# Kernel optimization log

Measured on AMD Instinct MI355X. Metric: run time of the kernel, lower is better.

The kernel has to match this reference:

```python
import jax, jax.numpy as jnp
import numpy as np

B, S, D, H, F, M = 2, 2048, 1024, 16, 4096, 1024
HD = D // H
LR, MOM_DECAY, WD, THRESH = 0.01, 0.9, 0.01, 0.1


def rmsnorm(x, w, eps=1e-8):
    n = jnp.linalg.norm(x, axis=-1, keepdims=True) * (x.shape[-1] ** -0.5)
    return w * x / (n + eps)


def rope_sin_cos(seq_len, dim):
    inv_freq = 1.0 / (10000.0 ** (jnp.arange(0, dim, 2, dtype=jnp.float32) / dim))
    ang = jnp.arange(seq_len, dtype=jnp.float32)[:, None] * inv_freq[None, :]  # [S, dim/2]
    return jnp.sin(ang), jnp.cos(ang)


def apply_rope(x, sin, cos):
    # x: [B,H,S,hd]; sin/cos: [S,hd/2] broadcast. Matches torch source:
    # split even/odd lanes, then CONCATENATE halves (not interleave).
    x1, x2 = x[..., ::2], x[..., 1::2]
    return jnp.concatenate([x1 * cos - x2 * sin, x1 * sin + x2 * cos], axis=-1)


def lmm_mlp(z, w0, b0, w1, b1):
    return jnp.maximum(z @ w0 + b0, 0.0) @ w1 + b1


def setup_inputs() -> dict:
    key = jax.random.key(0)
    k = jax.random.split(key, 20)
    sc = 0.02
    r = lambda i, shape: jax.random.normal(k[i], shape, jnp.float32) * sc
    return {
        'x': jax.random.normal(k[0], (B, S, D), jnp.float32),
        'mask': jnp.tril(jnp.ones((1, 1, S, S), dtype=bool)),
        'wq': r(1, (D, D)), 'wk': r(2, (D, D)), 'wv': r(3, (D, D)), 'wo': r(4, (D, D)),
        'n1': jnp.ones(D, jnp.float32), 'n2': jnp.ones(D, jnp.float32), 'n3': jnp.ones(D, jnp.float32),
        'ffn_w1': r(5, (D, F)), 'ffn_w2': r(6, (D, F)), 'ffn_w3': r(7, (F, D)),
        'pk_w': r(8, (D, M)), 'pk_b': jnp.zeros(M, jnp.float32),
        'pv_w': r(9, (D, M)), 'pv_b': jnp.zeros(M, jnp.float32),
        'pq_w': r(10, (D, M)), 'pq_b': jnp.zeros(M, jnp.float32),
        'l0_w': r(11, (M, M)), 'l0_b': jnp.zeros(M, jnp.float32),
        'l1_w': r(12, (M, M)), 'l1_b': jnp.zeros(M, jnp.float32),
        'm0_w': jnp.zeros((M, M), jnp.float32), 'm0_b': jnp.zeros(M, jnp.float32),
        'm1_w': jnp.zeros((M, M), jnp.float32), 'm1_b': jnp.zeros(M, jnp.float32),
    }


def reference(x, mask, wq, wk, wv, wo, n1, n2, n3, ffn_w1, ffn_w2, ffn_w3,
              pk_w, pk_b, pv_w, pv_b, pq_w, pq_b,
              l0_w, l0_b, l1_w, l1_b, m0_w, m0_b, m1_w, m1_b):
    # ---- attention sublayer (pre-norm, RoPE) ----
    hn = rmsnorm(x, n1)
    q = (hn @ wq).reshape(B, S, H, HD).transpose(0, 2, 1, 3)
    kk = (hn @ wk).reshape(B, S, H, HD).transpose(0, 2, 1, 3)
    v = (hn @ wv).reshape(B, S, H, HD).transpose(0, 2, 1, 3)
    sin, cos = rope_sin_cos(S, HD)
    q = apply_rope(q, sin, cos)
    kk = apply_rope(kk, sin, cos)
    scores = jnp.einsum('bhqd,bhkd->bhqk', q, kk) / np.sqrt(HD).astype(np.float32)
    scores = jnp.where(mask, scores, -jnp.inf)
    attn = jax.nn.softmax(scores, axis=-1)
    o = jnp.einsum('bhqk,bhkd->bhqd', attn, v).transpose(0, 2, 1, 3).reshape(B, S, D)
    h = x + o @ wo

    # ---- neural memory sublayer ----
    hn2 = rmsnorm(h, n2)
    q_lmm = hn2 @ pq_w + pq_b
    retrieved = lmm_mlp(q_lmm, l0_w, l0_b, l1_w, l1_b)  # uses PRE-update params

    # online Titan-style LMM update (torch does this under no_grad, after retrieval)
    kf = jax.lax.stop_gradient((hn2 @ pk_w + pk_b).reshape(B * S, M))
    vf = jax.lax.stop_gradient((hn2 @ pv_w + pv_b).reshape(B * S, M))

    def lmm_loss(params):
        pred = lmm_mlp(kf, *params)
        return jnp.sum(jnp.mean((pred - vf) ** 2, axis=-1))

    params = (l0_w, l0_b, l1_w, l1_b)
    loss_sum, grads = jax.value_and_grad(lmm_loss)(params)
    avg_loss = loss_sum / (B * S)
    do_update = avg_loss >= THRESH
    moms = (m0_w, m0_b, m1_w, m1_b)
    new_moms, new_params = [], []
    for p, m, g in zip(params, moms, grads):
        nm = MOM_DECAY * m - LR * g
        np_ = p * (1.0 - WD) + nm
        new_moms.append(jnp.where(do_update, nm, m))
        new_params.append(jnp.where(do_update, np_, p))

    h = h + retrieved

    # ---- SwiGLU FFN sublayer ----
    hn3 = rmsnorm(h, n3)
    ffn = (jax.nn.silu(hn3 @ ffn_w1) * (hn3 @ ffn_w2)) @ ffn_w3
    out = h + ffn
    return (out, *new_params, *new_moms)
```

## Files before the change

kernel.cpp:

```cpp
#include <hip/hip_runtime.h>
#include <cstdint>
#include <cstddef>

typedef __bf16 bf16;
typedef __bf16 bf16x2 __attribute__((ext_vector_type(2)));
typedef __bf16 bf16x4 __attribute__((ext_vector_type(4)));
typedef __bf16 bf16x8 __attribute__((ext_vector_type(8)));
typedef float  f32x4  __attribute__((ext_vector_type(4)));
typedef __attribute__((address_space(1))) unsigned int u32_g;
typedef __attribute__((address_space(3))) unsigned int u32_l;

#define DI __device__ __forceinline__

constexpr int Bc = 2, Sc = 2048, Dc = 1024, Hc = 16, HDc = 64, Fc = 4096, Mc = 1024;
constexpr int NTc = Bc * Sc;

DI void llds16(const bf16* g, bf16* l) {
  __builtin_amdgcn_global_load_lds((const u32_g*)g, (u32_l*)l, 16, 0, 0);
}
DI f32x4 cvt4(bf16x4 a) {
  f32x4 r; r[0] = (float)a[0]; r[1] = (float)a[1]; r[2] = (float)a[2]; r[3] = (float)a[3];
  return r;
}

__global__ void k_detect(const unsigned short* __restrict__ x, int* __restrict__ flag)
{
  const int tid = threadIdx.x;
  int cnt = 0;
#pragma unroll
  for (int i = 0; i < 8; i++) {
    unsigned short h = x[tid * 8 + i];
    int e = (h >> 7) & 0xFF;
    if (e < 96 || e > 160) cnt++;
  }
#pragma unroll
  for (int off = 32; off > 0; off >>= 1) cnt += __shfl_down(cnt, off, 64);
  if (tid == 0) *flag = (cnt > 32) ? 1 : 0;
}

__global__ __launch_bounds__(256)
void k_cvt(const void* __restrict__ src, bf16* __restrict__ dst, int n4, const int* __restrict__ flag)
{
  int i = blockIdx.x * 256 + threadIdx.x;
  if (i >= n4) return;
  bf16x4 o;
  if (*flag) {
    f32x4 v = ((const f32x4*)src)[i];
    o[0] = (bf16)v[0]; o[1] = (bf16)v[1]; o[2] = (bf16)v[2]; o[3] = (bf16)v[3];
  } else {
    o = ((const bf16x4*)src)[i];
  }
  ((bf16x4*)dst)[i] = o;
}

__global__ void k_transpose_dt(const void* __restrict__ src, bf16* __restrict__ dst,
                               int R, int C, const int* __restrict__ flag)
{
  __shared__ bf16 tile[32][33];
  const int c0 = blockIdx.x * 32, r0 = blockIdx.y * 32;
  const int tx = threadIdx.x, ty = threadIdx.y;
  const bool f32 = (*flag != 0);
  for (int i = ty; i < 32; i += 8) {
    size_t idx = (size_t)(r0 + i) * C + (c0 + tx);
    tile[i][tx] = f32 ? (bf16)((const float*)src)[idx] : ((const bf16*)src)[idx];
  }
  __syncthreads();
  for (int i = ty; i < 32; i += 8)
    dst[(size_t)(c0 + i) * R + (r0 + tx)] = tile[tx][i];
}

__global__ void k_transpose_v(const bf16* __restrict__ v, bf16* __restrict__ vt)
{
  __shared__ bf16 tile[32][33];
  const int d0 = blockIdx.x * 32, s0 = blockIdx.y * 32;
  const int bh = blockIdx.z;
  const int b = bh >> 4, hh = bh & 15;
  const int tx = threadIdx.x, ty = threadIdx.y;
  for (int i = ty; i < 32; i += 8)
    tile[i][tx] = v[((size_t)(b * Sc + s0 + i)) * Dc + hh * HDc + d0 + tx];
  __syncthreads();
  for (int i = ty; i < 32; i += 8)
    vt[((size_t)(bh * HDc + d0 + i)) * Sc + s0 + tx] = tile[tx][i];
}

enum EpiMode { EPI_BF16 = 0, EPI_BIAS_BF16, EPI_BIAS_RELU_BF16, EPI_BIAS_RESB_F32,
               EPI_SILU_BF16, EPI_DZ_BF16, EPI_RESX_BF16, EPI_RESF_F32 };

template <int EPI>
__global__ __launch_bounds__(256)
void k_gemm(const bf16* __restrict__ A, const bf16* __restrict__ Bt,
            int Mr, int Nr, int Kr,
            float* outF, bf16* outB,
            const bf16* __restrict__ bias, const bf16* auxB,
            const float* resF,
            const void* __restrict__ resX, const int* __restrict__ flag)
{
  __shared__ bf16 As[128 * 32];
  __shared__ bf16 Bs[128 * 32];
  const int tid = threadIdx.x;
  const int w = tid >> 6, l = tid & 63;
  const int wr = w >> 1, wc = w & 1;
  const int row0 = blockIdx.y * 128, col0 = blockIdx.x * 128;

  const f32x4 vzero = {0.f, 0.f, 0.f, 0.f};
  f32x4 acc[4][4];
#pragma unroll
  for (int i = 0; i < 4; i++)
#pragma unroll
    for (int j = 0; j < 4; j++) acc[i][j] = vzero;

  const bf16* Ag = A + (size_t)(row0 + w * 16 + (l >> 2)) * Kr + ((l & 3) << 3);
  const bf16* Bg = Bt + (size_t)(col0 + w * 16 + (l >> 2)) * Kr + ((l & 3) << 3);
  bf16* AsW = &As[w * 512];
  bf16* BsW = &Bs[w * 512];
  const size_t rowHop = (size_t)64 * Kr;

  for (int k0 = 0; k0 < Kr; k0 += 32) {
    __syncthreads();
    llds16(Ag + k0, AsW);
    llds16(Ag + rowHop + k0, AsW + 2048);
    llds16(Bg + k0, BsW);
    llds16(Bg + rowHop + k0, BsW + 2048);
    __syncthreads();
    bf16x8 af[4], bfr[4];
#pragma unroll
    for (int mt = 0; mt < 4; mt++)
      af[mt] = *(const bf16x8*)&As[(wr * 64 + mt * 16 + (l & 15)) * 32 + (l >> 4) * 8];
#pragma unroll
    for (int nt = 0; nt < 4; nt++)
      bfr[nt] = *(const bf16x8*)&Bs[(wc * 64 + nt * 16 + (l & 15)) * 32 + (l >> 4) * 8];
#pragma unroll
    for (int mt = 0; mt < 4; mt++)
#pragma unroll
      for (int nt = 0; nt < 4; nt++)
        acc[mt][nt] = __builtin_amdgcn_mfma_f32_16x16x32_bf16(af[mt], bfr[nt], acc[mt][nt], 0, 0, 0);
  }

  const bool f32res = (EPI == EPI_RESX_BF16) ? (*flag != 0) : false;
  float biasv[4];
  if (EPI == EPI_BIAS_BF16 || EPI == EPI_BIAS_RELU_BF16 || EPI == EPI_BIAS_RESB_F32) {
#pragma unroll
    for (int nt = 0; nt < 4; nt++)
      biasv[nt] = (float)bias[col0 + wc * 64 + nt * 16 + (l & 15)];
  }
#pragma unroll
  for (int mt = 0; mt < 4; mt++) {
    const int rowb = row0 + wr * 64 + mt * 16 + ((l >> 4) << 2);
    float av[4][4];
    if (EPI == EPI_SILU_BF16 || EPI == EPI_DZ_BF16 || EPI == EPI_BIAS_RESB_F32) {
#pragma unroll
      for (int nt = 0; nt < 4; nt++) {
        const int col = col0 + wc * 64 + nt * 16 + (l & 15);
#pragma unroll
        for (int r = 0; r < 4; r++)
          av[nt][r] = (float)auxB[(size_t)(rowb + r) * Nr + col];
      }
    }
    if (EPI == EPI_RESF_F32) {
#pragma unroll
      for (int nt = 0; nt < 4; nt++) {
        const int col = col0 + wc * 64 + nt * 16 + (l & 15);
#pragma unroll
        for (int r = 0; r < 4; r++)
          av[nt][r] = resF[(size_t)(rowb + r) * Nr + col];
      }
    }
    if (EPI == EPI_RESX_BF16) {
#pragma unroll
      for (int nt = 0; nt < 4; nt++) {
        const int col = col0 + wc * 64 + nt * 16 + (l & 15);
#pragma unroll
        for (int r = 0; r < 4; r++) {
          const size_t idx = (size_t)(rowb + r) * Nr + col;
          av[nt][r] = f32res ? ((const float*)resX)[idx] : (float)((const bf16*)resX)[idx];
        }
      }
    }
#pragma unroll
    for (int nt = 0; nt < 4; nt++) {
      const int col = col0 + wc * 64 + nt * 16 + (l & 15);
#pragma unroll
      for (int r = 0; r < 4; r++) {
        const size_t idx = (size_t)(rowb + r) * Nr + col;
        float v = acc[mt][nt][r];
        if (EPI == EPI_BF16) { outB[idx] = (bf16)v; }
        else if (EPI == EPI_BIAS_BF16) { outB[idx] = (bf16)(v + biasv[nt]); }
        else if (EPI == EPI_BIAS_RELU_BF16) { outB[idx] = (bf16)fmaxf(v + biasv[nt], 0.f); }
        else if (EPI == EPI_BIAS_RESB_F32) { outF[idx] = v + biasv[nt] + av[nt][r]; }
        else if (EPI == EPI_SILU_BF16) {
          float s1v = av[nt][r];
          float sl = s1v / (1.f + __expf(-s1v));
          outB[idx] = (bf16)(sl * v);
        }
        else if (EPI == EPI_DZ_BF16) { outB[idx] = (bf16)(av[nt][r] > 0.f ? v : 0.f); }
        else if (EPI == EPI_RESX_BF16) { outB[idx] = (bf16)(v + av[nt][r]); }
        else if (EPI == EPI_RESF_F32) { outF[idx] = v + av[nt][r]; }
      }
    }
  }
}

__global__ __launch_bounds__(256)
void k_gemm_tn(const bf16* __restrict__ X, const bf16* __restrict__ Y, int Kt,
               float* __restrict__ out)
{
  __shared__ bf16 As[128 * 36];
  __shared__ bf16 Bs[128 * 36];
  const int tid = threadIdx.x;
  const int w = tid >> 6, l = tid & 63;
  const int wr = w >> 1, wc = w & 1;
  const int row0 = blockIdx.y * 128, col0 = blockIdx.x * 128;
  const int iofs = (tid & 15) * 8;
  const int tp   = (tid >> 4) * 2;

  const f32x4 vzero = {0.f, 0.f, 0.f, 0.f};
  f32x4 acc[4][4];
#pragma unroll
  for (int i = 0; i < 4; i++)
#pragma unroll
    for (int j = 0; j < 4; j++) acc[i][j] = vzero;

  const int chunk = Kt / gridDim.z;
  const int tbeg = blockIdx.z * chunk;

  for (int t0 = tbeg; t0 < tbeg + chunk; t0 += 32) {
    __syncthreads();
    bf16x8 a0 = *(const bf16x8*)&X[(size_t)(t0 + tp) * 1024 + row0 + iofs];
    bf16x8 a1 = *(const bf16x8*)&X[(size_t)(t0 + tp + 1) * 1024 + row0 + iofs];
    bf16x8 b0 = *(const bf16x8*)&Y[(size_t)(t0 + tp) * 1024 + col0 + iofs];
    bf16x8 b1 = *(const bf16x8*)&Y[(size_t)(t0 + tp + 1) * 1024 + col0 + iofs];
#pragma unroll
    for (int e = 0; e < 8; e++) {
      bf16x2 pa; pa[0] = a0[e]; pa[1] = a1[e];
      bf16x2 pb; pb[0] = b0[e]; pb[1] = b1[e];
      *(bf16x2*)&As[(iofs + e) * 36 + tp] = pa;
      *(bf16x2*)&Bs[(iofs + e) * 36 + tp] = pb;
    }
    __syncthreads();
    bf16x8 af[4], bfr[4];
#pragma unroll
    for (int mt = 0; mt < 4; mt++) {
      const int base = (wr * 64 + mt * 16 + (l & 15)) * 36 + (l >> 4) * 8;
      bf16x4 lo = *(const bf16x4*)&As[base];
      bf16x4 hi = *(const bf16x4*)&As[base + 4];
#pragma unroll
      for (int e = 0; e < 4; e++) { af[mt][e] = lo[e]; af[mt][4 + e] = hi[e]; }
    }
#pragma unroll
    for (int nt = 0; nt < 4; nt++) {
      const int base = (wc * 64 + nt * 16 + (l & 15)) * 36 + (l >> 4) * 8;
      bf16x4 lo = *(const bf16x4*)&Bs[base];
      bf16x4 hi = *(const bf16x4*)&Bs[base + 4];
#pragma unroll
      for (int e = 0; e < 4; e++) { bfr[nt][e] = lo[e]; bfr[nt][4 + e] = hi[e]; }
    }
#pragma unroll
    for (int mt = 0; mt < 4; mt++)
#pragma unroll
      for (int nt = 0; nt < 4; nt++)
        acc[mt][nt] = __builtin_amdgcn_mfma_f32_16x16x32_bf16(af[mt], bfr[nt], acc[mt][nt], 0, 0, 0);
  }

#pragma unroll
  for (int mt = 0; mt < 4; mt++) {
    const int rowb = row0 + wr * 64 + mt * 16 + ((l >> 4) << 2);
#pragma unroll
    for (int nt = 0; nt < 4; nt++) {
      const int col = col0 + wc * 64 + nt * 16 + (l & 15);
#pragma unroll
      for (int r = 0; r < 4; r++)
        atomicAdd(&out[(size_t)(rowb + r) * 1024 + col], acc[mt][nt][r]);
    }
  }
}

__global__ __launch_bounds__(256)
void k_rmsnorm_dt(const void* __restrict__ x, const bf16* __restrict__ w, bf16* __restrict__ out,
                  const int* __restrict__ flag)
{
  const int row = blockIdx.x;
  const int tid = threadIdx.x;
  f32x4 xv;
  if (*flag) xv = *(const f32x4*)((const float*)x + (size_t)row * Dc + tid * 4);
  else       xv = cvt4(*(const bf16x4*)((const bf16*)x + (size_t)row * Dc + tid * 4));
  float ss = xv[0] * xv[0] + xv[1] * xv[1] + xv[2] * xv[2] + xv[3] * xv[3];
#pragma unroll
  for (int off = 32; off > 0; off >>= 1) ss += __shfl_down(ss, off, 64);
  __shared__ float part[4];
  if ((tid & 63) == 0) part[tid >> 6] = ss;
  __syncthreads();
  float tot = part[0] + part[1] + part[2] + part[3];
  float inv = 1.f / (sqrtf(tot) * 0.03125f + 1e-8f);
  bf16x4 wb = *(const bf16x4*)(w + tid * 4);
  bf16x4 ov;
  ov[0] = (bf16)((float)wb[0] * xv[0] * inv);
  ov[1] = (bf16)((float)wb[1] * xv[1] * inv);
  ov[2] = (bf16)((float)wb[2] * xv[2] * inv);
  ov[3] = (bf16)((float)wb[3] * xv[3] * inv);
  *(bf16x4*)(out + (size_t)row * Dc + tid * 4) = ov;
}

__global__ __launch_bounds__(256)
void k_rmsnorm_b(const bf16* __restrict__ x, const bf16* __restrict__ w, bf16* __restrict__ out)
{
  const int row = blockIdx.x;
  const int tid = threadIdx.x;
  f32x4 xv = cvt4(*(const bf16x4*)(x + (size_t)row * Dc + tid * 4));
  float ss = xv[0] * xv[0] + xv[1] * xv[1] + xv[2] * xv[2] + xv[3] * xv[3];
#pragma unroll
  for (int off = 32; off > 0; off >>= 1) ss += __shfl_down(ss, off, 64);
  __shared__ float part[4];
  if ((tid & 63) == 0) part[tid >> 6] = ss;
  __syncthreads();
  float tot = part[0] + part[1] + part[2] + part[3];
  float inv = 1.f / (sqrtf(tot) * 0.03125f + 1e-8f);
  bf16x4 wb = *(const bf16x4*)(w + tid * 4);
  bf16x4 ov;
  ov[0] = (bf16)((float)wb[0] * xv[0] * inv);
  ov[1] = (bf16)((float)wb[1] * xv[1] * inv);
  ov[2] = (bf16)((float)wb[2] * xv[2] * inv);
  ov[3] = (bf16)((float)wb[3] * xv[3] * inv);
  *(bf16x4*)(out + (size_t)row * Dc + tid * 4) = ov;
}

__global__ __launch_bounds__(256)
void k_rmsnorm_f(const float* __restrict__ x, const bf16* __restrict__ w, bf16* __restrict__ out)
{
  const int row = blockIdx.x;
  const int tid = threadIdx.x;
  f32x4 xv = *(const f32x4*)(x + (size_t)row * Dc + tid * 4);
  float ss = xv[0] * xv[0] + xv[1] * xv[1] + xv[2] * xv[2] + xv[3] * xv[3];
#pragma unroll
  for (int off = 32; off > 0; off >>= 1) ss += __shfl_down(ss, off, 64);
  __shared__ float part[4];
  if ((tid & 63) == 0) part[tid >> 6] = ss;
  __syncthreads();
  float tot = part[0] + part[1] + part[2] + part[3];
  float inv = 1.f / (sqrtf(tot) * 0.03125f + 1e-8f);
  bf16x4 wb = *(const bf16x4*)(w + tid * 4);
  bf16x4 ov;
  ov[0] = (bf16)((float)wb[0] * xv[0] * inv);
  ov[1] = (bf16)((float)wb[1] * xv[1] * inv);
  ov[2] = (bf16)((float)wb[2] * xv[2] * inv);
  ov[3] = (bf16)((float)wb[3] * xv[3] * inv);
  *(bf16x4*)(out + (size_t)row * Dc + tid * 4) = ov;
}

__global__ __launch_bounds__(256)
void k_rope(bf16* __restrict__ q, bf16* __restrict__ kx)
{
  const int idx = blockIdx.x * 256 + threadIdx.x;
  const int t = idx >> 4, hh = idx & 15;
  const int s = t & (Sc - 1);
  float sn[32], cs[32];
#pragma unroll
  for (int i = 0; i < 32; i++) {
    float f = expf(-(float)i * 0.28782313662425574f);
    float ang = (float)s * f;
    sn[i] = sinf(ang);
    cs[i] = cosf(ang);
  }
  for (int pass = 0; pass < 2; pass++) {
    bf16* p = (pass ? kx : q) + (size_t)t * Dc + hh * HDc;
    float xb[64], ob[64];
#pragma unroll
    for (int j = 0; j < 16; j++) *(f32x4*)&xb[j * 4] = cvt4(*(const bf16x4*)(p + j * 4));
#pragma unroll
    for (int i = 0; i < 32; i++) {
      float x1 = xb[2 * i], x2 = xb[2 * i + 1];
      ob[i] = x1 * cs[i] - x2 * sn[i];
      ob[32 + i] = x1 * sn[i] + x2 * cs[i];
    }
#pragma unroll
    for (int j = 0; j < 16; j++) {
      bf16x4 o4;
      o4[0] = (bf16)ob[j * 4]; o4[1] = (bf16)ob[j * 4 + 1];
      o4[2] = (bf16)ob[j * 4 + 2]; o4[3] = (bf16)ob[j * 4 + 3];
      *(bf16x4*)(p + j * 4) = o4;
    }
  }
}

__global__ __launch_bounds__(256)
void k_attn(const bf16* __restrict__ q, const bf16* __restrict__ kx,
            const bf16* __restrict__ vt, bf16* __restrict__ o)
{
  constexpr int PAD = 72;
  __shared__ bf16 Ps[4][16 * PAD];

  const int blk = blockIdx.x;
  const int qt = 31 - (blk >> 5);
  const int bh = blk & 31;
  const int b = bh >> 4, hh = bh & 15;
  const int tid = threadIdx.x;
  const int w = tid >> 6, l = tid & 63;
  const int quad = l >> 4, c = l & 15;

  const int qrow = qt * 64 + w * 16 + c;
  const size_t qbase = ((size_t)(b * Sc + qrow)) * Dc + hh * HDc;
  bf16x8 qf0 = *(const bf16x8*)(q + qbase + quad * 8);
  bf16x8 qf1 = *(const bf16x8*)(q + qbase + 32 + quad * 8);
#pragma unroll
  for (int j = 0; j < 8; j++) {
    qf0[j] = (bf16)((float)qf0[j] * 0.125f);
    qf1[j] = (bf16)((float)qf1[j] * 0.125f);
  }

  const f32x4 vzero = {0.f, 0.f, 0.f, 0.f};
  f32x4 oacc[4];
#pragma unroll
  for (int nt = 0; nt < 4; nt++) oacc[nt] = vzero;
  float mrun[4] = {-3.0e38f, -3.0e38f, -3.0e38f, -3.0e38f};
  float lrun[4] = {0.f, 0.f, 0.f, 0.f};

  const int qrow0 = qt * 64 + w * 16 + quad * 4;

  const bf16* kb = kx + (size_t)b * Sc * Dc + hh * HDc;
  const bf16* vb = vt + (size_t)bh * HDc * Sc;

  for (int t0 = 0; t0 <= qt; t0++) {
    const int kk0 = t0 * 64;

    f32x4 sf[4];
#pragma unroll
    for (int nt = 0; nt < 4; nt++) {
      const bf16* kr = kb + (size_t)(kk0 + nt * 16 + c) * Dc + quad * 8;
      bf16x8 k0 = *(const bf16x8*)kr;
      bf16x8 k1 = *(const bf16x8*)(kr + 32);
      f32x4 a = vzero;
      a = __builtin_amdgcn_mfma_f32_16x16x32_bf16(qf0, k0, a, 0, 0, 0);
      a = __builtin_amdgcn_mfma_f32_16x16x32_bf16(qf1, k1, a, 0, 0, 0);
      sf[nt] = a;
    }
    if (t0 == qt) {
#pragma unroll
      for (int nt = 0; nt < 4; nt++)
#pragma unroll
        for (int r = 0; r < 4; r++)
          if (kk0 + nt * 16 + c > qrow0 + r) sf[nt][r] = -3.0e38f;
    }

    float mnew[4], alpha[4];
#pragma unroll
    for (int r = 0; r < 4; r++) {
      float mt = fmaxf(fmaxf(sf[0][r], sf[1][r]), fmaxf(sf[2][r], sf[3][r]));
      mt = fmaxf(mt, __shfl_xor(mt, 1, 64));
      mt = fmaxf(mt, __shfl_xor(mt, 2, 64));
      mt = fmaxf(mt, __shfl_xor(mt, 4, 64));
      mt = fmaxf(mt, __shfl_xor(mt, 8, 64));
      mnew[r] = fmaxf(mrun[r], mt);
      alpha[r] = __expf(mrun[r] - mnew[r]);
      mrun[r] = mnew[r];
    }
    float ps[4] = {0.f, 0.f, 0.f, 0.f};
#pragma unroll
    for (int nt = 0; nt < 4; nt++)
#pragma unroll
      for (int r = 0; r < 4; r++) {
        float p = __expf(sf[nt][r] - mnew[r]);
        sf[nt][r] = p;
        ps[r] += p;
      }
#pragma unroll
    for (int r = 0; r < 4; r++) {
      ps[r] += __shfl_xor(ps[r], 1, 64);
      ps[r] += __shfl_xor(ps[r], 2, 64);
      ps[r] += __shfl_xor(ps[r], 4, 64);
      ps[r] += __shfl_xor(ps[r], 8, 64);
      lrun[r] = lrun[r] * alpha[r] + ps[r];
    }
#pragma unroll
    for (int nt = 0; nt < 4; nt++)
#pragma unroll
      for (int r = 0; r < 4; r++) oacc[nt][r] *= alpha[r];

#pragma unroll
    for (int nt = 0; nt < 4; nt++)
#pragma unroll
      for (int r = 0; r < 4; r++)
        Ps[w][(quad * 4 + r) * PAD + nt * 16 + c] = (bf16)sf[nt][r];
    bf16x8 pa0 = *(const bf16x8*)&Ps[w][c * PAD + quad * 8];
    bf16x8 pa1 = *(const bf16x8*)&Ps[w][c * PAD + 32 + quad * 8];

#pragma unroll
    for (int nt = 0; nt < 4; nt++) {
      const bf16* vr = vb + (size_t)(nt * 16 + c) * Sc + kk0 + quad * 8;
      bf16x8 v0 = *(const bf16x8*)vr;
      bf16x8 v1 = *(const bf16x8*)(vr + 32);
      oacc[nt] = __builtin_amdgcn_mfma_f32_16x16x32_bf16(pa0, v0, oacc[nt], 0, 0, 0);
      oacc[nt] = __builtin_amdgcn_mfma_f32_16x16x32_bf16(pa1, v1, oacc[nt], 0, 0, 0);
    }
  }

  float inv[4];
#pragma unroll
  for (int r = 0; r < 4; r++) inv[r] = 1.f / lrun[r];
#pragma unroll
  for (int r = 0; r < 4; r++) {
    const size_t obase = ((size_t)(b * Sc + qrow0 + r)) * Dc + hh * HDc;
#pragma unroll
    for (int nt = 0; nt < 4; nt++)
      o[obase + nt * 16 + c] = (bf16)(oacc[nt][r] * inv[r]);
  }
}

__global__ __launch_bounds__(256)
void k_relu(const bf16* __restrict__ src, bf16* __restrict__ dst)
{
  int i = blockIdx.x * 256 + threadIdx.x;
  bf16x8 v = ((const bf16x8*)src)[i];
  bf16x8 o;
#pragma unroll
  for (int e = 0; e < 8; e++) o[e] = ((float)v[e] > 0.f) ? v[e] : (bf16)0.f;
  ((bf16x8*)dst)[i] = o;
}

__global__ __launch_bounds__(256)
void k_dpred(bf16* __restrict__ predDp, const bf16* __restrict__ vf, float* __restrict__ loss)
{
  __shared__ float red[4];
  const int tid = threadIdx.x;
  const size_t n8 = (size_t)NTc * Mc / 8;
  float lacc = 0.f;
  for (size_t i = (size_t)blockIdx.x * 256 + tid; i < n8; i += (size_t)gridDim.x * 256) {
    bf16x8 p8 = ((const bf16x8*)predDp)[i];
    bf16x8 v8 = ((const bf16x8*)vf)[i];
    bf16x8 d8;
#pragma unroll
    for (int e = 0; e < 8; e++) {
      float df = (float)p8[e] - (float)v8[e];
      lacc += df * df;
      d8[e] = (bf16)(df * (2.0f / 1024.0f));
    }
    ((bf16x8*)predDp)[i] = d8;
  }
#pragma unroll
  for (int off = 32; off > 0; off >>= 1) lacc += __shfl_down(lacc, off, 64);
  if ((tid & 63) == 0) red[tid >> 6] = lacc;
  __syncthreads();
  if (tid == 0) atomicAdd(loss, red[0] + red[1] + red[2] + red[3]);
}

__global__ __launch_bounds__(256)
void k_colsum(const bf16* __restrict__ X, float* __restrict__ out, int C, int rowsPer)
{
  int c = blockIdx.x * 256 + threadIdx.x;
  int r0 = blockIdx.y * rowsPer;
  float s = 0.f;
#pragma unroll 8
  for (int r = r0; r < r0 + rowsPer; r++) s += (float)X[(size_t)r * C + c];
  atomicAdd(&out[c], s);
}

__global__ __launch_bounds__(256)
void k_update_dt(const void* __restrict__ p0w, const void* __restrict__ p0b,
                 const void* __restrict__ p1w, const void* __restrict__ p1b,
                 const void* __restrict__ m0w, const void* __restrict__ m0b,
                 const void* __restrict__ m1w, const void* __restrict__ m1b,
                 const float* __restrict__ g0wF, const float* __restrict__ g0b,
                 const float* __restrict__ g1wF, const float* __restrict__ g1b,
                 const float* __restrict__ loss, const int* __restrict__ flag,
                 float* __restrict__ outP, float* __restrict__ outM)
{
  const int i = blockIdx.x * 256 + threadIdx.x;
  const bool upd = (loss[0] >= 0.1f * 1024.f * 4096.f);
  const bool f32 = (*flag != 0);
  constexpr int W = 1024 * 1024;
  const void *pp, *pm; int j; float g;
  if (i < W) { pp = p0w; pm = m0w; j = i; g = g0wF[i]; }
  else if (i < W + 1024) { j = i - W; pp = p0b; pm = m0b; g = g0b[j]; }
  else if (i < 2 * W + 1024) { j = i - W - 1024; pp = p1w; pm = m1w; g = g1wF[j]; }
  else { j = i - 2 * W - 1024; pp = p1b; pm = m1b; g = g1b[j]; }
  float p = f32 ? ((const float*)pp)[j] : (float)((const bf16*)pp)[j];
  float m = f32 ? ((const float*)pm)[j] : (float)((const bf16*)pm)[j];
  float nm = 0.9f * m - 0.01f * g;
  float np = 0.99f * p + nm;
  outP[i] = upd ? np : p;
  outM[i] = upd ? nm : m;
}

extern "C" void kernel_launch(void* const* d_in, const int* in_sizes, int n_in,
                              void* d_out, int out_size, void* d_ws, size_t ws_size,
                              hipStream_t stream)
{
  (void)in_sizes; (void)n_in; (void)out_size; (void)ws_size;
  const void* x   = d_in[0];
  const void* wq  = d_in[2];
  const void* wk  = d_in[3];
  const void* wv  = d_in[4];
  const void* wo  = d_in[5];
  const void* n1  = d_in[6];
  const void* n2  = d_in[7];
  const void* n3  = d_in[8];
  const void* fw1 = d_in[9];
  const void* fw2 = d_in[10];
  const void* fw3 = d_in[11];
  const void* pkw = d_in[12];
  const void* pkb = d_in[13];
  const void* pvw = d_in[14];
  const void* pvb = d_in[15];
  const void* pqw = d_in[16];
  const void* pqb = d_in[17];
  const void* l0w = d_in[18];
  const void* l0b = d_in[19];
  const void* l1w = d_in[20];
  const void* l1b = d_in[21];
  const void* m0w = d_in[22];
  const void* m0b = d_in[23];
  const void* m1w = d_in[24];
  const void* m1b = d_in[25];

  char* ws = (char*)d_ws;
  size_t off = 0;
  auto alloc = [&](size_t bytes) -> char* {
    char* p = ws + off;
    off += (bytes + 255) & ~(size_t)255;
    return p;
  };

  const size_t DD = (size_t)Dc * Dc;
  const size_t ND = (size_t)NTc * Dc;
  const size_t MB8 = 2 * ND;
  const size_t M1 = DD;

  bf16* W = (bf16*)alloc(2 * 8 * M1);
  bf16 *wqT = W, *wkT = W + M1, *wvT = W + 2 * M1, *woT = W + 3 * M1;
  bf16 *pqT = W + 4 * M1, *pkT = W + 5 * M1, *pvT = W + 6 * M1, *l0T = W + 7 * M1;
  bf16 *l1T = W + M1;
  bf16 *l1c = W;
  bf16 *w1T = W + 4 * M1;
  bf16 *w2T = W;
  bf16 *w3T = W + 4 * M1;

  bf16* B0 = (bf16*)alloc(MB8);
  bf16* B1 = (bf16*)alloc(MB8);
  bf16* B2 = (bf16*)alloc(MB8);
  bf16* B3 = (bf16*)alloc(MB8);
  bf16* B4 = (bf16*)alloc(MB8);
  bf16* s1 = B0;
  bf16* VtG = B4;

  float* g0b = (float*)alloc(4 * 1024);
  float* g1b = (float*)alloc(4 * 1024);
  float* lossb = (float*)alloc(256);
  int*   flag  = (int*)alloc(256);
  bf16* n1c = (bf16*)alloc(2 * 1024);
  bf16* n2c = (bf16*)alloc(2 * 1024);
  bf16* n3c = (bf16*)alloc(2 * 1024);
  bf16* bqc = (bf16*)alloc(2 * 1024);
  bf16* bkc = (bf16*)alloc(2 * 1024);
  bf16* bvc = (bf16*)alloc(2 * 1024);
  bf16* b0c = (bf16*)alloc(2 * 1024);
  bf16* b1c = (bf16*)alloc(2 * 1024);

  float* outX = (float*)d_out;
  float* outP = outX + ND;
  float* outM = outP + (2 * DD + 2048);
  float* g0wF = outM;
  float* g1wF = outM + M1 + 1024;
  bf16*  hn   = (bf16*)outX;

  const dim3 tb(32, 8);

  hipMemsetAsync(lossb, 0, sizeof(float), stream);
  hipMemsetAsync(g0b, 0, 4 * 1024, stream);
  hipMemsetAsync(g1b, 0, 4 * 1024, stream);
  hipMemsetAsync(outM, 0, (2 * M1 + 2048) * sizeof(float), stream);
  k_detect<<<1, 64, 0, stream>>>((const unsigned short*)x, flag);

  k_cvt<<<1, 256, 0, stream>>>(n1, n1c, 256, flag);
  k_cvt<<<1, 256, 0, stream>>>(n2, n2c, 256, flag);
  k_cvt<<<1, 256, 0, stream>>>(n3, n3c, 256, flag);
  k_cvt<<<1, 256, 0, stream>>>(pqb, bqc, 256, flag);
  k_cvt<<<1, 256, 0, stream>>>(pkb, bkc, 256, flag);
  k_cvt<<<1, 256, 0, stream>>>(pvb, bvc, 256, flag);
  k_cvt<<<1, 256, 0, stream>>>(l0b, b0c, 256, flag);
  k_cvt<<<1, 256, 0, stream>>>(l1b, b1c, 256, flag);

  k_transpose_dt<<<dim3(32, 32), tb, 0, stream>>>(wq, wqT, Dc, Dc, flag);
  k_transpose_dt<<<dim3(32, 32), tb, 0, stream>>>(wk, wkT, Dc, Dc, flag);
  k_transpose_dt<<<dim3(32, 32), tb, 0, stream>>>(wv, wvT, Dc, Dc, flag);
  k_transpose_dt<<<dim3(32, 32), tb, 0, stream>>>(wo, woT, Dc, Dc, flag);
  k_transpose_dt<<<dim3(32, 32), tb, 0, stream>>>(pqw, pqT, Dc, Mc, flag);
  k_transpose_dt<<<dim3(32, 32), tb, 0, stream>>>(pkw, pkT, Dc, Mc, flag);
  k_transpose_dt<<<dim3(32, 32), tb, 0, stream>>>(pvw, pvT, Dc, Mc, flag);
  k_transpose_dt<<<dim3(32, 32), tb, 0, stream>>>(l0w, l0T, Mc, Mc, flag);

  k_rmsnorm_dt<<<NTc, 256, 0, stream>>>(x, n1c, hn, flag);
  k_gemm<EPI_BF16><<<dim3(8, 32), 256, 0, stream>>>(hn, wqT, NTc, Dc, Dc, nullptr, B0, nullptr, nullptr, nullptr, nullptr, nullptr);
  k_gemm<EPI_BF16><<<dim3(8, 32), 256, 0, stream>>>(hn, wkT, NTc, Dc, Dc, nullptr, B1, nullptr, nullptr, nullptr, nullptr, nullptr);
  k_gemm<EPI_BF16><<<dim3(8, 32), 256, 0, stream>>>(hn, wvT, NTc, Dc, Dc, nullptr, B2, nullptr, nullptr, nullptr, nullptr, nullptr);
  k_transpose_v<<<dim3(2, 64, 32), tb, 0, stream>>>(B2, VtG);
  k_rope<<<256, 256, 0, stream>>>(B0, B1);
  k_attn<<<1024, 256, 0, stream>>>(B0, B1, VtG, B3);
  k_gemm<EPI_RESX_BF16><<<dim3(8, 32), 256, 0, stream>>>(B3, woT, NTc, Dc, Dc, nullptr, B4, nullptr, nullptr, nullptr, x, flag);
  k_transpose_dt<<<dim3(32, 32), tb, 0, stream>>>(l1w, l1T, Mc, Mc, flag);

  k_rmsnorm_b<<<NTc, 256, 0, stream>>>(B4, n2c, B0);
  k_gemm<EPI_BIAS_BF16><<<dim3(8, 32), 256, 0, stream>>>(B0, pqT, NTc, Mc, Dc, nullptr, B1, bqc, nullptr, nullptr, nullptr, nullptr);
  k_gemm<EPI_BIAS_BF16><<<dim3(8, 32), 256, 0, stream>>>(B0, pkT, NTc, Mc, Dc, nullptr, B2, bkc, nullptr, nullptr, nullptr, nullptr);
  k_gemm<EPI_BIAS_BF16><<<dim3(8, 32), 256, 0, stream>>>(B0, pvT, NTc, Mc, Dc, nullptr, B3, bvc, nullptr, nullptr, nullptr, nullptr);
  k_gemm<EPI_BIAS_RELU_BF16><<<dim3(8, 32), 256, 0, stream>>>(B1, l0T, NTc, Mc, Mc, nullptr, B0, b0c, nullptr, nullptr, nullptr, nullptr);
  k_gemm<EPI_BIAS_RESB_F32><<<dim3(8, 32), 256, 0, stream>>>(B0, l1T, NTc, Mc, Mc, outX, nullptr, b1c, B4, nullptr, nullptr, nullptr);

  k_gemm<EPI_BIAS_BF16><<<dim3(8, 32), 256, 0, stream>>>(B2, l0T, NTc, Mc, Mc, nullptr, B4, b0c, nullptr, nullptr, nullptr, nullptr);
  k_transpose_dt<<<dim3(128, 32), tb, 0, stream>>>(fw1, w1T, Dc, Fc, flag);
  k_relu<<<2048, 256, 0, stream>>>(B4, B0);
  k_gemm<EPI_BIAS_BF16><<<dim3(8, 32), 256, 0, stream>>>(B0, l1T, NTc, Mc, Mc, nullptr, B1, b1c, nullptr, nullptr, nullptr, nullptr);
  k_cvt<<<1024, 256, 0, stream>>>(l1w, l1c, (int)(DD / 4), flag);
  k_dpred<<<256, 256, 0, stream>>>(B1, B3, lossb);
  k_gemm<EPI_DZ_BF16><<<dim3(8, 32), 256, 0, stream>>>(B1, l1c, NTc, Mc, Mc, nullptr, B3, nullptr, B4, nullptr, nullptr, nullptr);
  k_gemm_tn<<<dim3(8, 8, 8), 256, 0, stream>>>(B0, B1, NTc, g1wF);
  k_gemm_tn<<<dim3(8, 8, 8), 256, 0, stream>>>(B2, B3, NTc, g0wF);
  k_colsum<<<dim3(4, 32), 256, 0, stream>>>(B1, g1b, Mc, NTc / 32);
  k_colsum<<<dim3(4, 32), 256, 0, stream>>>(B3, g0b, Mc, NTc / 32);
  k_update_dt<<<8200, 256, 0, stream>>>(l0w, l0b, l1w, l1b, m0w, m0b, m1w, m1b,
                                        g0wF, g0b, g1wF, g1b, lossb, flag, outP, outM);

  k_transpose_dt<<<dim3(128, 32), tb, 0, stream>>>(fw2, w2T, Dc, Fc, flag);
  k_rmsnorm_f<<<NTc, 256, 0, stream>>>(outX, n3c, B4);
  k_gemm<EPI_BF16><<<dim3(32, 32), 256, 0, stream>>>(B4, w1T, NTc, Fc, Dc, nullptr, s1, nullptr, nullptr, nullptr, nullptr, nullptr);
  k_transpose_dt<<<dim3(32, 128), tb, 0, stream>>>(fw3, w3T, Fc, Dc, flag);
  k_gemm<EPI_SILU_BF16><<<dim3(32, 32), 256, 0, stream>>>(B4, w2T, NTc, Fc, Dc, nullptr, s1, nullptr, s1, nullptr, nullptr, nullptr);
  k_gemm<EPI_RESF_F32><<<dim3(8, 32), 256, 0, stream>>>(s1, w3T, NTc, Dc, Fc, outX, nullptr, nullptr, nullptr, outX, nullptr, nullptr);
}
```

Before: 1.117 ms.

## Split attention KV loop across waves with in-block softmax merge

Each attention block now handles 16 query rows instead of 64, and the four waves split the key tiles among themselves in strided order. Partial outputs, maxima and sums from waves 1-3 go through shared memory and are merged by wave 0 with a log-sum-exp rescale. The grid grows fourfold to raise parallelism and balance causal work. In exchange, waves in a block no longer share the same K/V tiles, so total K/V loads increase, and a merge step with two barriers is added.

```diff
diff --git a/kernel.cpp b/kernel.cpp
--- a/kernel.cpp
+++ b/kernel.cpp
@@ -386,17 +386,20 @@
             const bf16* __restrict__ vt, bf16* __restrict__ o)
 {
   constexpr int PAD = 72;
-  __shared__ bf16 Ps[4][16 * PAD];
+  __shared__ __align__(16) char smem[19456];
 
   const int blk = blockIdx.x;
-  const int qt = 31 - (blk >> 5);
+  const int qi = 127 - (blk >> 5);
   const int bh = blk & 31;
   const int b = bh >> 4, hh = bh & 15;
   const int tid = threadIdx.x;
   const int w = tid >> 6, l = tid & 63;
   const int quad = l >> 4, c = l & 15;
 
-  const int qrow = qt * 64 + w * 16 + c;
+  bf16* Psw = (bf16*)smem + w * 16 * PAD;
+  float* Buf = (float*)smem;
+
+  const int qrow = qi * 16 + c;
   const size_t qbase = ((size_t)(b * Sc + qrow)) * Dc + hh * HDc;
   bf16x8 qf0 = *(const bf16x8*)(q + qbase + quad * 8);
   bf16x8 qf1 = *(const bf16x8*)(q + qbase + 32 + quad * 8);
@@ -413,12 +416,13 @@
   float mrun[4] = {-3.0e38f, -3.0e38f, -3.0e38f, -3.0e38f};
   float lrun[4] = {0.f, 0.f, 0.f, 0.f};
 
-  const int qrow0 = qt * 64 + w * 16 + quad * 4;
+  const int qrow0 = qi * 16 + quad * 4;
+  const int ntiles = (qi >> 2) + 1;
 
   const bf16* kb = kx + (size_t)b * Sc * Dc + hh * HDc;
   const bf16* vb = vt + (size_t)bh * HDc * Sc;
 
-  for (int t0 = 0; t0 <= qt; t0++) {
+  for (int t0 = w; t0 < ntiles; t0 += 4) {
     const int kk0 = t0 * 64;
 
     f32x4 sf[4];
@@ -432,7 +436,7 @@
       a = __builtin_amdgcn_mfma_f32_16x16x32_bf16(qf1, k1, a, 0, 0, 0);
       sf[nt] = a;
     }
-    if (t0 == qt) {
+    if (t0 == ntiles - 1) {
 #pragma unroll
       for (int nt = 0; nt < 4; nt++)
 #pragma unroll
@@ -478,9 +482,9 @@
     for (int nt = 0; nt < 4; nt++)
 #pragma unroll
       for (int r = 0; r < 4; r++)
-        Ps[w][(quad * 4 + r) * PAD + nt * 16 + c] = (bf16)sf[nt][r];
-    bf16x8 pa0 = *(const bf16x8*)&Ps[w][c * PAD + quad * 8];
-    bf16x8 pa1 = *(const bf16x8*)&Ps[w][c * PAD + 32 + quad * 8];
+        Psw[(quad * 4 + r) * PAD + nt * 16 + c] = (bf16)sf[nt][r];
+    bf16x8 pa0 = *(const bf16x8*)&Psw[c * PAD + quad * 8];
+    bf16x8 pa1 = *(const bf16x8*)&Psw[c * PAD + 32 + quad * 8];
 
 #pragma unroll
     for (int nt = 0; nt < 4; nt++) {
@@ -492,15 +496,46 @@
     }
   }
 
-  float inv[4];
-#pragma unroll
-  for (int r = 0; r < 4; r++) inv[r] = 1.f / lrun[r];
-#pragma unroll
-  for (int r = 0; r < 4; r++) {
-    const size_t obase = ((size_t)(b * Sc + qrow0 + r)) * Dc + hh * HDc;
+  __syncthreads();
+  if (w > 0) {
+    float* dst = Buf + ((w - 1) * 64 + l) * 25;
 #pragma unroll
     for (int nt = 0; nt < 4; nt++)
-      o[obase + nt * 16 + c] = (bf16)(oacc[nt][r] * inv[r]);
+#pragma unroll
+      for (int r = 0; r < 4; r++) dst[nt * 4 + r] = oacc[nt][r];
+#pragma unroll
+    for (int r = 0; r < 4; r++) { dst[16 + r] = mrun[r]; dst[20 + r] = lrun[r]; }
+  }
+  __syncthreads();
+  if (w == 0) {
+#pragma unroll
+    for (int w2 = 0; w2 < 3; w2++) {
+      const float* src = Buf + (w2 * 64 + l) * 25;
+      float m2[4], l2[4];
+#pragma unroll
+      for (int r = 0; r < 4; r++) { m2[r] = src[16 + r]; l2[r] = src[20 + r]; }
+#pragma unroll
+      for (int r = 0; r < 4; r++) {
+        float mn = fmaxf(mrun[r], m2[r]);
+        float a = __expf(mrun[r] - mn);
+        float bb = __expf(m2[r] - mn);
+        lrun[r] = lrun[r] * a + l2[r] * bb;
+        mrun[r] = mn;
+#pragma unroll
+        for (int nt = 0; nt < 4; nt++)
+          oacc[nt][r] = oacc[nt][r] * a + src[nt * 4 + r] * bb;
+      }
+    }
+    float inv[4];
+#pragma unroll
+    for (int r = 0; r < 4; r++) inv[r] = 1.f / lrun[r];
+#pragma unroll
+    for (int r = 0; r < 4; r++) {
+      const size_t obase = ((size_t)(b * Sc + qrow0 + r)) * Dc + hh * HDc;
+#pragma unroll
+      for (int nt = 0; nt < 4; nt++)
+        o[obase + nt * 16 + c] = (bf16)(oacc[nt][r] * inv[r]);
+    }
   }
 }
 
@@ -692,7 +727,7 @@
   k_gemm<EPI_BF16><<<dim3(8, 32), 256, 0, stream>>>(hn, wvT, NTc, Dc, Dc, nullptr, B2, nullptr, nullptr, nullptr, nullptr, nullptr);
   k_transpose_v<<<dim3(2, 64, 32), tb, 0, stream>>>(B2, VtG);
   k_rope<<<256, 256, 0, stream>>>(B0, B1);
-  k_attn<<<1024, 256, 0, stream>>>(B0, B1, VtG, B3);
+  k_attn<<<4096, 256, 0, stream>>>(B0, B1, VtG, B3);
   k_gemm<EPI_RESX_BF16><<<dim3(8, 32), 256, 0, stream>>>(B3, woT, NTc, Dc, Dc, nullptr, B4, nullptr, nullptr, nullptr, x, flag);
   k_transpose_dt<<<dim3(32, 32), tb, 0, stream>>>(l1w, l1T, Mc, Mc, flag);
 
```

Result: faster. 1.091 ms (-2.3%).
